# Performance work log

Measured on AMD Instinct MI355X. Metric: run time of the kernel, lower is better.

The kernel has to match this reference:

```python
import jax, jax.numpy as jnp
import numpy as np

B, D, S = 8192, 1024, 32  # batch, feature dim, number of sessions (experts)


def setup_inputs() -> dict:
    key = jax.random.key(0)
    k1, k2, k3, k4 = jax.random.split(key, 4)
    x = jax.random.normal(k1, (B, D), dtype=jnp.float32)
    # Expert bank: original init is identity affine; perturb so the test is nontrivial.
    W = jnp.eye(D, dtype=jnp.float32)[None, :, :] + 0.02 * jax.random.normal(k2, (S, D, D), dtype=jnp.float32)
    b = 0.02 * jax.random.normal(k3, (S, D), dtype=jnp.float32)
    session_idx = jax.random.randint(k4, (B,), 0, S)  # int session id per sample
    return {"x": x, "W": W, "b": b, "session_idx": session_idx}


def reference(x, W, b, session_idx):
    """Per-sample session-affine dispatch: out[i] = W[session_idx[i]] @ x[i] + b[session_idx[i]].

    Implemented as a scan over the (small, fixed) set of S experts: one dense
    [B,D]x[D,D] GEMM per expert, masked-accumulated into the output. This avoids
    gathering a [B,D,D] per-sample weight tensor.
    """
    num_sessions = W.shape[0]

    def step(acc, packed):
        Ws, bs, s = packed                       # Ws: [D,D], bs: [D]
        y = x @ Ws.T + bs                        # [B,D] dense affine for expert s
        mask = (session_idx == s)[:, None]       # [B,1] samples belonging to s
        return acc + jnp.where(mask, y, jnp.zeros((), x.dtype)), None

    out, _ = jax.lax.scan(step, jnp.zeros_like(x), (W, b, jnp.arange(num_sessions)))
    return out
```

## Files before the change

kernel.cpp:

```cpp
#include <hip/hip_runtime.h>
#include <cstddef>

#define B_ROWS 8192
#define DIM    1024
#define NSESS  32
#define MT     128
#define NTILE  128
#define BK     64
#define KITERS (DIM / BK)
#define TPE    3
#define LROW   72
#define TSZ    (MT * LROW)
#define NXCD   8
#define EPX    (NSESS / NXCD)
#define BPE    (TPE * (DIM / NTILE))

typedef __attribute__((ext_vector_type(8))) short short8;
typedef __attribute__((ext_vector_type(4))) float floatx4;
typedef __attribute__((ext_vector_type(4))) int intx4;
typedef __attribute__((ext_vector_type(2))) unsigned int uintx2;

__device__ __forceinline__ unsigned pack_bf16_2(float fa, float fb) {
  unsigned a = __builtin_bit_cast(unsigned, fa);
  unsigned b = __builtin_bit_cast(unsigned, fb);
  a += 0x7fffu + ((a >> 16) & 1u);
  b += 0x7fffu + ((b >> 16) & 1u);
  return __builtin_amdgcn_perm(b, a, 0x07060302u);
}

__global__ __launch_bounds__(256, 3) void gemm_kernel(
    const float* __restrict__ x, const float* __restrict__ W,
    const float* __restrict__ bias, const int* __restrict__ sidx,
    float* __restrict__ out)
{
  __shared__ __align__(16) short As[TSZ], Bs[TSZ];
  __shared__ int row_ids[MT];
  __shared__ int psum[256];

  const int hw    = blockIdx.x;
  const int xcd   = hw & (NXCD - 1);
  const int r     = hw >> 3;
  const int s     = xcd * EPX + (r / BPE);
  const int rr    = r % BPE;
  const int ntile = rr / TPE;
  const int mtile = rr % TPE;
  const int tid   = threadIdx.x;

  const int lane = tid & 63;
  const int wv   = tid >> 6;
  const int wm   = wv >> 1;
  const int wn   = wv & 1;
  const int fr   = lane & 15;
  const int kg   = lane >> 4;

  const int srow   = wv * 32 + (lane >> 4);
  const int schunk = lane & 15;

  unsigned boff[8];
  floatx4 wreg[8];
  {
    const unsigned wbyte =
        (unsigned)(((size_t)s * DIM * DIM + (size_t)(ntile * NTILE) * DIM) * 4u);
#pragma unroll
    for (int j = 0; j < 8; ++j) {
      const int tr = srow + j * 4;
      boff[j] = wbyte + (unsigned)((tr * DIM + schunk * 4) * 4);
      wreg[j] = *(const floatx4*)((const char*)W + boff[j]);
    }
  }

  const intx4* sv = (const intx4*)(sidx + tid * 32);
  int c = 0;
#pragma unroll
  for (int j = 0; j < 8; ++j) {
    const intx4 v = sv[j];
#pragma unroll
    for (int e = 0; e < 4; ++e) c += (v[e] == s);
  }
  psum[tid] = c;
  __syncthreads();
#pragma unroll
  for (int d = 1; d < 256; d <<= 1) {
    const int mine = psum[tid];
    const int add  = (tid >= d) ? psum[tid - d] : 0;
    __syncthreads();
    psum[tid] = mine + add;
    __syncthreads();
  }
  const int total = psum[255];
  const int nrows = (total - mtile * MT) < 0 ? 0
                  : ((total - mtile * MT) > MT ? MT : (total - mtile * MT));
  if (nrows == 0) return;
  const int base_rank = psum[tid] - c;

  if (tid < MT) row_ids[tid] = -1;
  __syncthreads();
  {
    int r2 = base_rank;
    const int lo = mtile * MT, hi = lo + MT;
#pragma unroll
    for (int j = 0; j < 8; ++j) {
      const intx4 v = sv[j];
#pragma unroll
      for (int e = 0; e < 4; ++e) {
        if (v[e] == s) {
          if (r2 >= lo && r2 < hi) row_ids[r2 - lo] = tid * 32 + 4 * j + e;
          ++r2;
        }
      }
    }
  }
  __syncthreads();

  unsigned aoff[8];
  floatx4 xreg[8];
#pragma unroll
  for (int j = 0; j < 8; ++j) {
    int ar = row_ids[srow + j * 4];
    if (ar < 0) ar = 0;
    aoff[j] = (unsigned)((ar * DIM + schunk * 4) * 4);
    xreg[j] = *(const floatx4*)((const char*)x + aoff[j]);
  }

  floatx4 acc[4][4] = {};

#define LOADREGS(KB)                                                           \
  {                                                                            \
    _Pragma("unroll")                                                          \
    for (int j = 0; j < 8; ++j) {                                              \
      xreg[j] = *(const floatx4*)((const char*)x + aoff[j] + (KB) * (BK * 4)); \
      wreg[j] = *(const floatx4*)((const char*)W + boff[j] + (KB) * (BK * 4)); \
    }                                                                          \
  }

#define CVTWRITE()                                                             \
  {                                                                            \
    _Pragma("unroll")                                                          \
    for (int j = 0; j < 8; ++j) {                                              \
      const int off = (srow + j * 4) * LROW + schunk * 4;                      \
      uintx2 ua = { pack_bf16_2(xreg[j][0], xreg[j][1]),                       \
                    pack_bf16_2(xreg[j][2], xreg[j][3]) };                     \
      uintx2 ub = { pack_bf16_2(wreg[j][0], wreg[j][1]),                       \
                    pack_bf16_2(wreg[j][2], wreg[j][3]) };                     \
      *(uintx2*)&As[off] = ua;                                                 \
      *(uintx2*)&Bs[off] = ub;                                                 \
    }                                                                          \
  }

#define COMPUTE()                                                              \
  {                                                                            \
    _Pragma("unroll")                                                          \
    for (int s2 = 0; s2 < 2; ++s2) {                                           \
      short8 fb[4];                                                            \
      _Pragma("unroll")                                                        \
      for (int i = 0; i < 4; ++i)                                              \
        fb[i] = *(const short8*)&Bs[(wn * 64 + i * 16 + fr) * LROW + s2 * 32 + kg * 8]; \
      _Pragma("unroll")                                                        \
      for (int mi = 0; mi < 4; ++mi) {                                         \
        const short8 fa = *(const short8*)&As[(wm * 64 + mi * 16 + fr) * LROW + s2 * 32 + kg * 8]; \
        _Pragma("unroll")                                                      \
        for (int ni = 0; ni < 4; ++ni)                                         \
          acc[mi][ni] = __builtin_amdgcn_mfma_f32_16x16x32_bf16(               \
              fa, fb[ni], acc[mi][ni], 0, 0, 0);                               \
      }                                                                        \
    }                                                                          \
  }

  CVTWRITE();
  __syncthreads();

  for (int kb = 0; kb < KITERS; ++kb) {
    if (kb + 1 < KITERS) LOADREGS(kb + 1);
    COMPUTE();
    if (kb + 1 < KITERS) {
      __syncthreads();
      CVTWRITE();
      __syncthreads();
    }
  }

#undef LOADREGS
#undef CVTWRITE
#undef COMPUTE

  const int col0 = ntile * NTILE + wn * 64;
#pragma unroll
  for (int ni = 0; ni < 4; ++ni) {
    const int n = col0 + ni * 16 + fr;
    const float bv = bias[s * DIM + n];
#pragma unroll
    for (int mi = 0; mi < 4; ++mi) {
      const int mbase = wm * 64 + mi * 16 + kg * 4;
#pragma unroll
      for (int rr2 = 0; rr2 < 4; ++rr2) {
        const int ml = mbase + rr2;
        if (ml < nrows) {
          const int orow = row_ids[ml];
          out[(size_t)orow * DIM + n] = acc[mi][ni][rr2] + bv;
        }
      }
    }
  }
}

extern "C" void kernel_launch(void* const* d_in, const int* in_sizes, int n_in,
                              void* d_out, int out_size, void* d_ws, size_t ws_size,
                              hipStream_t stream) {
  const float* x    = (const float*)d_in[0];
  const float* W    = (const float*)d_in[1];
  const float* b    = (const float*)d_in[2];
  const int*   sidx = (const int*)d_in[3];
  float* out = (float*)d_out;
  (void)d_ws; (void)ws_size;

  hipLaunchKernelGGL(gemm_kernel, dim3(NSESS * TPE * (DIM / NTILE)), dim3(256), 0, stream,
                     x, W, b, sidx, out);
}
```

Baseline: 280.5 us.

## Pre-convert x and W to bf16 in workspace before the session GEMM

Adds a grid-stride kernel that converts x and the expert weight bank from fp32 to bf16 into the workspace. A new GEMM variant then loads bf16 tiles directly and copies them to shared memory without converting in the main loop. The aim is to halve the bytes the GEMM streams from memory, since each W tile is re-read by several m-tile blocks, and to remove per-iteration conversion work. In exchange it adds two launches and a full extra read and write pass over the 128 MB weight bank on every call. The original fp32 path is kept as a fallback when the workspace is too small.

```diff
diff --git a/kernel.cpp b/kernel.cpp
--- a/kernel.cpp
+++ b/kernel.cpp
@@ -15,10 +15,14 @@
 #define EPX    (NSESS / NXCD)
 #define BPE    (TPE * (DIM / NTILE))
 
+#define XB_BYTES ((size_t)B_ROWS * DIM * 2)
+#define WB_BYTES ((size_t)NSESS * DIM * DIM * 2)
+
 typedef __attribute__((ext_vector_type(8))) short short8;
 typedef __attribute__((ext_vector_type(4))) float floatx4;
 typedef __attribute__((ext_vector_type(4))) int intx4;
 typedef __attribute__((ext_vector_type(2))) unsigned int uintx2;
+typedef __attribute__((ext_vector_type(4))) unsigned int uintx4;
 
 __device__ __forceinline__ unsigned pack_bf16_2(float fa, float fb) {
   unsigned a = __builtin_bit_cast(unsigned, fa);
@@ -28,8 +32,22 @@
   return __builtin_amdgcn_perm(b, a, 0x07060302u);
 }
 
-__global__ __launch_bounds__(256, 3) void gemm_kernel(
-    const float* __restrict__ x, const float* __restrict__ W,
+
+__global__ __launch_bounds__(256) void cvt_bf16_kernel(
+    const float* __restrict__ src, unsigned short* __restrict__ dst, int n8)
+{
+  const int stride = gridDim.x * blockDim.x;
+  for (int i = blockIdx.x * blockDim.x + threadIdx.x; i < n8; i += stride) {
+    const floatx4 a = ((const floatx4*)src)[2 * i];
+    const floatx4 b = ((const floatx4*)src)[2 * i + 1];
+    uintx4 o = { pack_bf16_2(a[0], a[1]), pack_bf16_2(a[2], a[3]),
+                 pack_bf16_2(b[0], b[1]), pack_bf16_2(b[2], b[3]) };
+    *(uintx4*)(dst + (size_t)i * 8) = o;
+  }
+}
+
+__global__ __launch_bounds__(256, 3) void gemm_kernel_bf16(
+    const unsigned short* __restrict__ xb, const unsigned short* __restrict__ wb,
     const float* __restrict__ bias, const int* __restrict__ sidx,
     float* __restrict__ out)
 {
@@ -53,19 +71,18 @@
   const int fr   = lane & 15;
   const int kg   = lane >> 4;
 
-  const int srow   = wv * 32 + (lane >> 4);
-  const int schunk = lane & 15;
-
-  unsigned boff[8];
-  floatx4 wreg[8];
+  const int srow8 = wv * 32 + (lane >> 3);
+  const int sch   = lane & 7;
+
+  unsigned boff[4];
+  short8 wr[4];
   {
-    const unsigned wbyte =
-        (unsigned)(((size_t)s * DIM * DIM + (size_t)(ntile * NTILE) * DIM) * 4u);
-#pragma unroll
-    for (int j = 0; j < 8; ++j) {
-      const int tr = srow + j * 4;
-      boff[j] = wbyte + (unsigned)((tr * DIM + schunk * 4) * 4);
-      wreg[j] = *(const floatx4*)((const char*)W + boff[j]);
+    const unsigned wbyte = (unsigned)s * (unsigned)(DIM * DIM * 2)
+                         + (unsigned)(ntile * NTILE) * (unsigned)(DIM * 2);
+#pragma unroll
+    for (int j = 0; j < 4; ++j) {
+      boff[j] = wbyte + (unsigned)((srow8 + j * 8) * (DIM * 2) + sch * 16);
+      wr[j] = *(const short8*)((const char*)wb + boff[j]);
     }
   }
 
@@ -112,14 +129,14 @@
   }
   __syncthreads();
 
-  unsigned aoff[8];
-  floatx4 xreg[8];
-#pragma unroll
-  for (int j = 0; j < 8; ++j) {
-    int ar = row_ids[srow + j * 4];
+  unsigned aoff[4];
+  short8 xr[4];
+#pragma unroll
+  for (int j = 0; j < 4; ++j) {
+    int ar = row_ids[srow8 + j * 8];
     if (ar < 0) ar = 0;
-    aoff[j] = (unsigned)((ar * DIM + schunk * 4) * 4);
-    xreg[j] = *(const floatx4*)((const char*)x + aoff[j]);
+    aoff[j] = (unsigned)(ar * (DIM * 2) + sch * 16);
+    xr[j] = *(const short8*)((const char*)xb + aoff[j]);
   }
 
   floatx4 acc[4][4] = {};
@@ -127,23 +144,19 @@
 #define LOADREGS(KB)                                                           \
   {                                                                            \
     _Pragma("unroll")                                                          \
-    for (int j = 0; j < 8; ++j) {                                              \
-      xreg[j] = *(const floatx4*)((const char*)x + aoff[j] + (KB) * (BK * 4)); \
-      wreg[j] = *(const floatx4*)((const char*)W + boff[j] + (KB) * (BK * 4)); \
-    }                                                                          \
-  }
-
-#define CVTWRITE()                                                             \
-  {                                                                            \
-    _Pragma("unroll")                                                          \
-    for (int j = 0; j < 8; ++j) {                                              \
-      const int off = (srow + j * 4) * LROW + schunk * 4;                      \
-      uintx2 ua = { pack_bf16_2(xreg[j][0], xreg[j][1]),                       \
-                    pack_bf16_2(xreg[j][2], xreg[j][3]) };                     \
-      uintx2 ub = { pack_bf16_2(wreg[j][0], wreg[j][1]),                       \
-                    pack_bf16_2(wreg[j][2], wreg[j][3]) };                     \
-      *(uintx2*)&As[off] = ua;                                                 \
-      *(uintx2*)&Bs[off] = ub;                                                 \
+    for (int j = 0; j < 4; ++j) {                                              \
+      xr[j] = *(const short8*)((const char*)xb + aoff[j] + (KB) * (BK * 2));   \
+      wr[j] = *(const short8*)((const char*)wb + boff[j] + (KB) * (BK * 2));   \
+    }                                                                          \
+  }
+
+#define DSWRITE()                                                              \
+  {                                                                            \
+    _Pragma("unroll")                                                          \
+    for (int j = 0; j < 4; ++j) {                                              \
+      const int off = (srow8 + j * 8) * LROW + sch * 8;                        \
+      *(short8*)&As[off] = xr[j];                                              \
+      *(short8*)&Bs[off] = wr[j];                                              \
     }                                                                          \
   }
 
@@ -166,6 +179,181 @@
     }                                                                          \
   }
 
+  DSWRITE();
+  __syncthreads();
+
+  for (int kb = 0; kb < KITERS; ++kb) {
+    if (kb + 1 < KITERS) LOADREGS(kb + 1);
+    COMPUTE();
+    if (kb + 1 < KITERS) {
+      __syncthreads();
+      DSWRITE();
+      __syncthreads();
+    }
+  }
+
+#undef LOADREGS
+#undef DSWRITE
+#undef COMPUTE
+
+  const int col0 = ntile * NTILE + wn * 64;
+#pragma unroll
+  for (int ni = 0; ni < 4; ++ni) {
+    const int n = col0 + ni * 16 + fr;
+    const float bv = bias[s * DIM + n];
+#pragma unroll
+    for (int mi = 0; mi < 4; ++mi) {
+      const int mbase = wm * 64 + mi * 16 + kg * 4;
+#pragma unroll
+      for (int rr2 = 0; rr2 < 4; ++rr2) {
+        const int ml = mbase + rr2;
+        if (ml < nrows) {
+          const int orow = row_ids[ml];
+          out[(size_t)orow * DIM + n] = acc[mi][ni][rr2] + bv;
+        }
+      }
+    }
+  }
+}
+
+__global__ __launch_bounds__(256, 3) void gemm_kernel(
+    const float* __restrict__ x, const float* __restrict__ W,
+    const float* __restrict__ bias, const int* __restrict__ sidx,
+    float* __restrict__ out)
+{
+  __shared__ __align__(16) short As[TSZ], Bs[TSZ];
+  __shared__ int row_ids[MT];
+  __shared__ int psum[256];
+
+  const int hw    = blockIdx.x;
+  const int xcd   = hw & (NXCD - 1);
+  const int r     = hw >> 3;
+  const int s     = xcd * EPX + (r / BPE);
+  const int rr    = r % BPE;
+  const int ntile = rr / TPE;
+  const int mtile = rr % TPE;
+  const int tid   = threadIdx.x;
+
+  const int lane = tid & 63;
+  const int wv   = tid >> 6;
+  const int wm   = wv >> 1;
+  const int wn   = wv & 1;
+  const int fr   = lane & 15;
+  const int kg   = lane >> 4;
+
+  const int srow   = wv * 32 + (lane >> 4);
+  const int schunk = lane & 15;
+
+  unsigned boff[8];
+  floatx4 wreg[8];
+  {
+    const unsigned wbyte =
+        (unsigned)(((size_t)s * DIM * DIM + (size_t)(ntile * NTILE) * DIM) * 4u);
+#pragma unroll
+    for (int j = 0; j < 8; ++j) {
+      const int tr = srow + j * 4;
+      boff[j] = wbyte + (unsigned)((tr * DIM + schunk * 4) * 4);
+      wreg[j] = *(const floatx4*)((const char*)W + boff[j]);
+    }
+  }
+
+  const intx4* sv = (const intx4*)(sidx + tid * 32);
+  int c = 0;
+#pragma unroll
+  for (int j = 0; j < 8; ++j) {
+    const intx4 v = sv[j];
+#pragma unroll
+    for (int e = 0; e < 4; ++e) c += (v[e] == s);
+  }
+  psum[tid] = c;
+  __syncthreads();
+#pragma unroll
+  for (int d = 1; d < 256; d <<= 1) {
+    const int mine = psum[tid];
+    const int add  = (tid >= d) ? psum[tid - d] : 0;
+    __syncthreads();
+    psum[tid] = mine + add;
+    __syncthreads();
+  }
+  const int total = psum[255];
+  const int nrows = (total - mtile * MT) < 0 ? 0
+                  : ((total - mtile * MT) > MT ? MT : (total - mtile * MT));
+  if (nrows == 0) return;
+  const int base_rank = psum[tid] - c;
+
+  if (tid < MT) row_ids[tid] = -1;
+  __syncthreads();
+  {
+    int r2 = base_rank;
+    const int lo = mtile * MT, hi = lo + MT;
+#pragma unroll
+    for (int j = 0; j < 8; ++j) {
+      const intx4 v = sv[j];
+#pragma unroll
+      for (int e = 0; e < 4; ++e) {
+        if (v[e] == s) {
+          if (r2 >= lo && r2 < hi) row_ids[r2 - lo] = tid * 32 + 4 * j + e;
+          ++r2;
+        }
+      }
+    }
+  }
+  __syncthreads();
+
+  unsigned aoff[8];
+  floatx4 xreg[8];
+#pragma unroll
+  for (int j = 0; j < 8; ++j) {
+    int ar = row_ids[srow + j * 4];
+    if (ar < 0) ar = 0;
+    aoff[j] = (unsigned)((ar * DIM + schunk * 4) * 4);
+    xreg[j] = *(const floatx4*)((const char*)x + aoff[j]);
+  }
+
+  floatx4 acc[4][4] = {};
+
+#define LOADREGS(KB)                                                           \
+  {                                                                            \
+    _Pragma("unroll")                                                          \
+    for (int j = 0; j < 8; ++j) {                                              \
+      xreg[j] = *(const floatx4*)((const char*)x + aoff[j] + (KB) * (BK * 4)); \
+      wreg[j] = *(const floatx4*)((const char*)W + boff[j] + (KB) * (BK * 4)); \
+    }                                                                          \
+  }
+
+#define CVTWRITE()                                                             \
+  {                                                                            \
+    _Pragma("unroll")                                                          \
+    for (int j = 0; j < 8; ++j) {                                              \
+      const int off = (srow + j * 4) * LROW + schunk * 4;                      \
+      uintx2 ua = { pack_bf16_2(xreg[j][0], xreg[j][1]),                       \
+                    pack_bf16_2(xreg[j][2], xreg[j][3]) };                     \
+      uintx2 ub = { pack_bf16_2(wreg[j][0], wreg[j][1]),                       \
+                    pack_bf16_2(wreg[j][2], wreg[j][3]) };                     \
+      *(uintx2*)&As[off] = ua;                                                 \
+      *(uintx2*)&Bs[off] = ub;                                                 \
+    }                                                                          \
+  }
+
+#define COMPUTE()                                                              \
+  {                                                                            \
+    _Pragma("unroll")                                                          \
+    for (int s2 = 0; s2 < 2; ++s2) {                                           \
+      short8 fb[4];                                                            \
+      _Pragma("unroll")                                                        \
+      for (int i = 0; i < 4; ++i)                                              \
+        fb[i] = *(const short8*)&Bs[(wn * 64 + i * 16 + fr) * LROW + s2 * 32 + kg * 8]; \
+      _Pragma("unroll")                                                        \
+      for (int mi = 0; mi < 4; ++mi) {                                         \
+        const short8 fa = *(const short8*)&As[(wm * 64 + mi * 16 + fr) * LROW + s2 * 32 + kg * 8]; \
+        _Pragma("unroll")                                                      \
+        for (int ni = 0; ni < 4; ++ni)                                         \
+          acc[mi][ni] = __builtin_amdgcn_mfma_f32_16x16x32_bf16(               \
+              fa, fb[ni], acc[mi][ni], 0, 0, 0);                               \
+      }                                                                        \
+    }                                                                          \
+  }
+
   CVTWRITE();
   __syncthreads();
 
@@ -211,8 +399,18 @@
   const float* b    = (const float*)d_in[2];
   const int*   sidx = (const int*)d_in[3];
   float* out = (float*)d_out;
-  (void)d_ws; (void)ws_size;
-
-  hipLaunchKernelGGL(gemm_kernel, dim3(NSESS * TPE * (DIM / NTILE)), dim3(256), 0, stream,
-                     x, W, b, sidx, out);
+
+  if (d_ws && ws_size >= XB_BYTES + WB_BYTES) {
+    unsigned short* xb = (unsigned short*)d_ws;
+    unsigned short* wb = xb + (size_t)B_ROWS * DIM;
+    hipLaunchKernelGGL(cvt_bf16_kernel, dim3(1024), dim3(256), 0, stream,
+                       x, xb, B_ROWS * DIM / 8);
+    hipLaunchKernelGGL(cvt_bf16_kernel, dim3(2048), dim3(256), 0, stream,
+                       W, wb, NSESS * DIM * DIM / 8);
+    hipLaunchKernelGGL(gemm_kernel_bf16, dim3(NSESS * TPE * (DIM / NTILE)),
+                       dim3(256), 0, stream, xb, wb, b, sidx, out);
+  } else {
+    hipLaunchKernelGGL(gemm_kernel, dim3(NSESS * TPE * (DIM / NTILE)),
+                       dim3(256), 0, stream, x, W, b, sidx, out);
+  }
 }
```

Result: no change. 281.4 us (+0.3%).

## Enlarge GEMM tile to 256x256 with 512-thread blocks and BK=32

Applied to the files above, without the earlier changes.

Retiles the per-session GEMM from 128x128 output tiles with 256 threads to 256x256 tiles with 512 threads (8 waves, 2x4 layout, each wave computing 128x64), halving BK to 32 to keep shared memory small. Rows per session are now covered by two M-tiles instead of three, so each weight tile is loaded fewer times and per-block arithmetic intensity rises. The trade-off is fewer blocks (256 instead of 768), more accumulator registers per thread, twice as many K iterations each with two barriers, and a longer 512-wide prefix scan. The kernel also assumes no session has more than 512 rows, the same kind of bound the 3x128 tiling had.

```diff
diff --git a/kernel.cpp b/kernel.cpp
--- a/kernel.cpp
+++ b/kernel.cpp
@@ -4,12 +4,12 @@
 #define B_ROWS 8192
 #define DIM    1024
 #define NSESS  32
-#define MT     128
-#define NTILE  128
-#define BK     64
+#define MT     256
+#define NTILE  256
+#define BK     32
 #define KITERS (DIM / BK)
-#define TPE    3
-#define LROW   72
+#define TPE    2
+#define LROW   40
 #define TSZ    (MT * LROW)
 #define NXCD   8
 #define EPX    (NSESS / NXCD)
@@ -28,51 +28,50 @@
   return __builtin_amdgcn_perm(b, a, 0x07060302u);
 }
 
-__global__ __launch_bounds__(256, 3) void gemm_kernel(
+__global__ __launch_bounds__(512, 2) void gemm_kernel(
     const float* __restrict__ x, const float* __restrict__ W,
     const float* __restrict__ bias, const int* __restrict__ sidx,
     float* __restrict__ out)
 {
   __shared__ __align__(16) short As[TSZ], Bs[TSZ];
   __shared__ int row_ids[MT];
-  __shared__ int psum[256];
+  __shared__ int psum[512];
 
   const int hw    = blockIdx.x;
   const int xcd   = hw & (NXCD - 1);
   const int r     = hw >> 3;
   const int s     = xcd * EPX + (r / BPE);
   const int rr    = r % BPE;
-  const int ntile = rr / TPE;
-  const int mtile = rr % TPE;
+  const int ntile = rr >> 1;
+  const int mtile = rr & 1;
   const int tid   = threadIdx.x;
 
   const int lane = tid & 63;
   const int wv   = tid >> 6;
-  const int wm   = wv >> 1;
-  const int wn   = wv & 1;
+  const int wm   = wv >> 2;
+  const int wn   = wv & 3;
   const int fr   = lane & 15;
   const int kg   = lane >> 4;
 
-  const int srow   = wv * 32 + (lane >> 4);
-  const int schunk = lane & 15;
-
-  unsigned boff[8];
-  floatx4 wreg[8];
+  const int srow = tid >> 3;
+  const int sch  = tid & 7;
+
+  unsigned boff[4];
+  floatx4 wr[4];
   {
     const unsigned wbyte =
         (unsigned)(((size_t)s * DIM * DIM + (size_t)(ntile * NTILE) * DIM) * 4u);
 #pragma unroll
-    for (int j = 0; j < 8; ++j) {
-      const int tr = srow + j * 4;
-      boff[j] = wbyte + (unsigned)((tr * DIM + schunk * 4) * 4);
-      wreg[j] = *(const floatx4*)((const char*)W + boff[j]);
-    }
-  }
-
-  const intx4* sv = (const intx4*)(sidx + tid * 32);
+    for (int j = 0; j < 4; ++j) {
+      boff[j] = wbyte + (unsigned)(((srow + j * 64) * DIM + sch * 4) * 4);
+      wr[j] = *(const floatx4*)((const char*)W + boff[j]);
+    }
+  }
+
+  const intx4* sv = (const intx4*)(sidx + tid * 16);
   int c = 0;
 #pragma unroll
-  for (int j = 0; j < 8; ++j) {
+  for (int j = 0; j < 4; ++j) {
     const intx4 v = sv[j];
 #pragma unroll
     for (int e = 0; e < 4; ++e) c += (v[e] == s);
@@ -80,14 +79,14 @@
   psum[tid] = c;
   __syncthreads();
 #pragma unroll
-  for (int d = 1; d < 256; d <<= 1) {
+  for (int d = 1; d < 512; d <<= 1) {
     const int mine = psum[tid];
     const int add  = (tid >= d) ? psum[tid - d] : 0;
     __syncthreads();
     psum[tid] = mine + add;
     __syncthreads();
   }
-  const int total = psum[255];
+  const int total = psum[511];
   const int nrows = (total - mtile * MT) < 0 ? 0
                   : ((total - mtile * MT) > MT ? MT : (total - mtile * MT));
   if (nrows == 0) return;
@@ -99,12 +98,12 @@
     int r2 = base_rank;
     const int lo = mtile * MT, hi = lo + MT;
 #pragma unroll
-    for (int j = 0; j < 8; ++j) {
+    for (int j = 0; j < 4; ++j) {
       const intx4 v = sv[j];
 #pragma unroll
       for (int e = 0; e < 4; ++e) {
         if (v[e] == s) {
-          if (r2 >= lo && r2 < hi) row_ids[r2 - lo] = tid * 32 + 4 * j + e;
+          if (r2 >= lo && r2 < hi) row_ids[r2 - lo] = tid * 16 + 4 * j + e;
           ++r2;
         }
       }
@@ -112,36 +111,36 @@
   }
   __syncthreads();
 
-  unsigned aoff[8];
-  floatx4 xreg[8];
-#pragma unroll
-  for (int j = 0; j < 8; ++j) {
-    int ar = row_ids[srow + j * 4];
+  unsigned aoff[4];
+  floatx4 xr[4];
+#pragma unroll
+  for (int j = 0; j < 4; ++j) {
+    int ar = row_ids[srow + j * 64];
     if (ar < 0) ar = 0;
-    aoff[j] = (unsigned)((ar * DIM + schunk * 4) * 4);
-    xreg[j] = *(const floatx4*)((const char*)x + aoff[j]);
-  }
-
-  floatx4 acc[4][4] = {};
+    aoff[j] = (unsigned)((ar * DIM + sch * 4) * 4);
+    xr[j] = *(const floatx4*)((const char*)x + aoff[j]);
+  }
+
+  floatx4 acc[8][4] = {};
 
 #define LOADREGS(KB)                                                           \
   {                                                                            \
     _Pragma("unroll")                                                          \
-    for (int j = 0; j < 8; ++j) {                                              \
-      xreg[j] = *(const floatx4*)((const char*)x + aoff[j] + (KB) * (BK * 4)); \
-      wreg[j] = *(const floatx4*)((const char*)W + boff[j] + (KB) * (BK * 4)); \
+    for (int j = 0; j < 4; ++j) {                                              \
+      xr[j] = *(const floatx4*)((const char*)x + aoff[j] + (KB) * (BK * 4));   \
+      wr[j] = *(const floatx4*)((const char*)W + boff[j] + (KB) * (BK * 4));   \
     }                                                                          \
   }
 
 #define CVTWRITE()                                                             \
   {                                                                            \
     _Pragma("unroll")                                                          \
-    for (int j = 0; j < 8; ++j) {                                              \
-      const int off = (srow + j * 4) * LROW + schunk * 4;                      \
-      uintx2 ua = { pack_bf16_2(xreg[j][0], xreg[j][1]),                       \
-                    pack_bf16_2(xreg[j][2], xreg[j][3]) };                     \
-      uintx2 ub = { pack_bf16_2(wreg[j][0], wreg[j][1]),                       \
-                    pack_bf16_2(wreg[j][2], wreg[j][3]) };                     \
+    for (int j = 0; j < 4; ++j) {                                              \
+      const int off = (srow + j * 64) * LROW + sch * 4;                        \
+      uintx2 ua = { pack_bf16_2(xr[j][0], xr[j][1]),                           \
+                    pack_bf16_2(xr[j][2], xr[j][3]) };                         \
+      uintx2 ub = { pack_bf16_2(wr[j][0], wr[j][1]),                           \
+                    pack_bf16_2(wr[j][2], wr[j][3]) };                         \
       *(uintx2*)&As[off] = ua;                                                 \
       *(uintx2*)&Bs[off] = ub;                                                 \
     }                                                                          \
@@ -149,20 +148,17 @@
 
 #define COMPUTE()                                                              \
   {                                                                            \
-    _Pragma("unroll")                                                          \
-    for (int s2 = 0; s2 < 2; ++s2) {                                           \
-      short8 fb[4];                                                            \
+    short8 fb[4];                                                              \
+    _Pragma("unroll")                                                          \
+    for (int i = 0; i < 4; ++i)                                                \
+      fb[i] = *(const short8*)&Bs[(wn * 64 + i * 16 + fr) * LROW + kg * 8];    \
+    _Pragma("unroll")                                                          \
+    for (int mi = 0; mi < 8; ++mi) {                                           \
+      const short8 fa = *(const short8*)&As[(wm * 128 + mi * 16 + fr) * LROW + kg * 8]; \
       _Pragma("unroll")                                                        \
-      for (int i = 0; i < 4; ++i)                                              \
-        fb[i] = *(const short8*)&Bs[(wn * 64 + i * 16 + fr) * LROW + s2 * 32 + kg * 8]; \
-      _Pragma("unroll")                                                        \
-      for (int mi = 0; mi < 4; ++mi) {                                         \
-        const short8 fa = *(const short8*)&As[(wm * 64 + mi * 16 + fr) * LROW + s2 * 32 + kg * 8]; \
-        _Pragma("unroll")                                                      \
-        for (int ni = 0; ni < 4; ++ni)                                         \
-          acc[mi][ni] = __builtin_amdgcn_mfma_f32_16x16x32_bf16(               \
-              fa, fb[ni], acc[mi][ni], 0, 0, 0);                               \
-      }                                                                        \
+      for (int ni = 0; ni < 4; ++ni)                                           \
+        acc[mi][ni] = __builtin_amdgcn_mfma_f32_16x16x32_bf16(                 \
+            fa, fb[ni], acc[mi][ni], 0, 0, 0);                                 \
     }                                                                          \
   }
 
@@ -189,8 +185,8 @@
     const int n = col0 + ni * 16 + fr;
     const float bv = bias[s * DIM + n];
 #pragma unroll
-    for (int mi = 0; mi < 4; ++mi) {
-      const int mbase = wm * 64 + mi * 16 + kg * 4;
+    for (int mi = 0; mi < 8; ++mi) {
+      const int mbase = wm * 128 + mi * 16 + kg * 4;
 #pragma unroll
       for (int rr2 = 0; rr2 < 4; ++rr2) {
         const int ml = mbase + rr2;
@@ -213,6 +209,6 @@
   float* out = (float*)d_out;
   (void)d_ws; (void)ws_size;
 
-  hipLaunchKernelGGL(gemm_kernel, dim3(NSESS * TPE * (DIM / NTILE)), dim3(256), 0, stream,
-                     x, W, b, sidx, out);
+  hipLaunchKernelGGL(gemm_kernel, dim3(NSESS * TPE * (DIM / NTILE)), dim3(512),
+                     0, stream, x, W, b, sidx, out);
 }
```

New measurement: 289.2 us. +3.1%, slower.

## Double-buffer LDS tiles and prefetch two K-steps ahead in registers

Applied to the files above, without the earlier changes.

Splits the shared-memory A/B tiles into two ping-pong buffers and keeps two register sets of prefetched global data, so the loop needs one barrier per K-step instead of two. While one LDS buffer feeds the MFMAs, the other is written with converted bf16 data, and global loads are issued two K-steps ahead. This doubles LDS use and register pressure, so launch bounds drop from 3 to 2 waves per EU, which cuts occupancy.

```diff
diff --git a/kernel.cpp b/kernel.cpp
--- a/kernel.cpp
+++ b/kernel.cpp
@@ -28,12 +28,13 @@
   return __builtin_amdgcn_perm(b, a, 0x07060302u);
 }
 
-__global__ __launch_bounds__(256, 3) void gemm_kernel(
+__global__ __launch_bounds__(256, 2) void gemm_kernel(
     const float* __restrict__ x, const float* __restrict__ W,
     const float* __restrict__ bias, const int* __restrict__ sidx,
     float* __restrict__ out)
 {
-  __shared__ __align__(16) short As[TSZ], Bs[TSZ];
+  __shared__ __align__(16) short As0[TSZ], As1[TSZ];
+  __shared__ __align__(16) short Bs0[TSZ], Bs1[TSZ];
   __shared__ int row_ids[MT];
   __shared__ int psum[256];
 
@@ -57,7 +58,7 @@
   const int schunk = lane & 15;
 
   unsigned boff[8];
-  floatx4 wreg[8];
+  floatx4 wr0[8], wr1[8];
   {
     const unsigned wbyte =
         (unsigned)(((size_t)s * DIM * DIM + (size_t)(ntile * NTILE) * DIM) * 4u);
@@ -65,8 +66,11 @@
     for (int j = 0; j < 8; ++j) {
       const int tr = srow + j * 4;
       boff[j] = wbyte + (unsigned)((tr * DIM + schunk * 4) * 4);
-      wreg[j] = *(const floatx4*)((const char*)W + boff[j]);
-    }
+      wr0[j] = *(const floatx4*)((const char*)W + boff[j]);
+    }
+#pragma unroll
+    for (int j = 0; j < 8; ++j)
+      wr1[j] = *(const floatx4*)((const char*)W + boff[j] + (BK * 4));
   }
 
   const intx4* sv = (const intx4*)(sidx + tid * 32);
@@ -113,51 +117,54 @@
   __syncthreads();
 
   unsigned aoff[8];
-  floatx4 xreg[8];
+  floatx4 xr0[8], xr1[8];
 #pragma unroll
   for (int j = 0; j < 8; ++j) {
     int ar = row_ids[srow + j * 4];
     if (ar < 0) ar = 0;
     aoff[j] = (unsigned)((ar * DIM + schunk * 4) * 4);
-    xreg[j] = *(const floatx4*)((const char*)x + aoff[j]);
-  }
+    xr0[j] = *(const floatx4*)((const char*)x + aoff[j]);
+  }
+#pragma unroll
+  for (int j = 0; j < 8; ++j)
+    xr1[j] = *(const floatx4*)((const char*)x + aoff[j] + (BK * 4));
 
   floatx4 acc[4][4] = {};
 
-#define LOADREGS(KB)                                                           \
+#define LOADSET(XR, WR, KB)                                                    \
   {                                                                            \
     _Pragma("unroll")                                                          \
     for (int j = 0; j < 8; ++j) {                                              \
-      xreg[j] = *(const floatx4*)((const char*)x + aoff[j] + (KB) * (BK * 4)); \
-      wreg[j] = *(const floatx4*)((const char*)W + boff[j] + (KB) * (BK * 4)); \
+      XR[j] = *(const floatx4*)((const char*)x + aoff[j] + (KB) * (BK * 4));   \
+      WR[j] = *(const floatx4*)((const char*)W + boff[j] + (KB) * (BK * 4));   \
     }                                                                          \
   }
 
-#define CVTWRITE()                                                             \
+#define CVTWRITE(XR, WR, AS, BS)                                               \
   {                                                                            \
     _Pragma("unroll")                                                          \
     for (int j = 0; j < 8; ++j) {                                              \
       const int off = (srow + j * 4) * LROW + schunk * 4;                      \
-      uintx2 ua = { pack_bf16_2(xreg[j][0], xreg[j][1]),                       \
-                    pack_bf16_2(xreg[j][2], xreg[j][3]) };                     \
-      uintx2 ub = { pack_bf16_2(wreg[j][0], wreg[j][1]),                       \
-                    pack_bf16_2(wreg[j][2], wreg[j][3]) };                     \
-      *(uintx2*)&As[off] = ua;                                                 \
-      *(uintx2*)&Bs[off] = ub;                                                 \
+      uintx2 ua = { pack_bf16_2(XR[j][0], XR[j][1]),                           \
+                    pack_bf16_2(XR[j][2], XR[j][3]) };                         \
+      uintx2 ub = { pack_bf16_2(WR[j][0], WR[j][1]),                           \
+                    pack_bf16_2(WR[j][2], WR[j][3]) };                         \
+      *(uintx2*)&AS[off] = ua;                                                 \
+      *(uintx2*)&BS[off] = ub;                                                 \
     }                                                                          \
   }
 
-#define COMPUTE()                                                              \
+#define COMPUTE(AS, BS)                                                        \
   {                                                                            \
     _Pragma("unroll")                                                          \
     for (int s2 = 0; s2 < 2; ++s2) {                                           \
       short8 fb[4];                                                            \
       _Pragma("unroll")                                                        \
       for (int i = 0; i < 4; ++i)                                              \
-        fb[i] = *(const short8*)&Bs[(wn * 64 + i * 16 + fr) * LROW + s2 * 32 + kg * 8]; \
+        fb[i] = *(const short8*)&BS[(wn * 64 + i * 16 + fr) * LROW + s2 * 32 + kg * 8]; \
       _Pragma("unroll")                                                        \
       for (int mi = 0; mi < 4; ++mi) {                                         \
-        const short8 fa = *(const short8*)&As[(wm * 64 + mi * 16 + fr) * LROW + s2 * 32 + kg * 8]; \
+        const short8 fa = *(const short8*)&AS[(wm * 64 + mi * 16 + fr) * LROW + s2 * 32 + kg * 8]; \
         _Pragma("unroll")                                                      \
         for (int ni = 0; ni < 4; ++ni)                                         \
           acc[mi][ni] = __builtin_amdgcn_mfma_f32_16x16x32_bf16(               \
@@ -166,20 +173,24 @@
     }                                                                          \
   }
 
-  CVTWRITE();
-  __syncthreads();
-
-  for (int kb = 0; kb < KITERS; ++kb) {
-    if (kb + 1 < KITERS) LOADREGS(kb + 1);
-    COMPUTE();
-    if (kb + 1 < KITERS) {
-      __syncthreads();
-      CVTWRITE();
-      __syncthreads();
-    }
-  }
-
-#undef LOADREGS
+  CVTWRITE(xr0, wr0, As0, Bs0);
+  __syncthreads();
+
+  for (int kb = 0; kb < KITERS; kb += 2) {
+    if (kb + 2 < KITERS) LOADSET(xr0, wr0, kb + 2);
+    COMPUTE(As0, Bs0);
+    CVTWRITE(xr1, wr1, As1, Bs1);
+    __syncthreads();
+
+    if (kb + 3 < KITERS) LOADSET(xr1, wr1, kb + 3);
+    COMPUTE(As1, Bs1);
+    if (kb + 2 < KITERS) {
+      CVTWRITE(xr0, wr0, As0, Bs0);
+    }
+    __syncthreads();
+  }
+
+#undef LOADSET
 #undef CVTWRITE
 #undef COMPUTE
 
@@ -213,6 +224,6 @@
   float* out = (float*)d_out;
   (void)d_ws; (void)ws_size;
 
-  hipLaunchKernelGGL(gemm_kernel, dim3(NSESS * TPE * (DIM / NTILE)), dim3(256), 0, stream,
-                     x, W, b, sidx, out);
+  hipLaunchKernelGGL(gemm_kernel, dim3(NSESS * TPE * (DIM / NTILE)), dim3(256),
+                     0, stream, x, W, b, sidx, out);
 }
```

New measurement: 386.8 us. 37.9% more time.
